# Optimization experiments

Measured on AMD Instinct MI355X. Metric: run time of the kernel, lower is better.

Reference implementation:

```python
import jax, jax.numpy as jnp
import numpy as np

N = 2048      # n_nodes
D = 512       # n_channels
AVG_DEG = 16  # average graph degree


def setup_inputs() -> dict:
    key = jax.random.key(0)
    k1, k2, k3 = jax.random.split(key, 3)
    # node features [N, D]
    x = jax.random.normal(k1, (N, D), dtype=jnp.float32)
    # random symmetric graph -> combinatorial Laplacian L = D - A
    E = N * AVG_DEG
    src = jax.random.randint(k2, (E,), 0, N)
    dst = jax.random.randint(k3, (E,), 0, N)
    A = jnp.zeros((N, N), jnp.float32).at[src, dst].add(1.0)
    A = (A + A.T) * 0.5
    A = A * (1.0 - jnp.eye(N, dtype=jnp.float32))  # drop self loops
    deg = A.sum(axis=1)
    L = jnp.diag(deg) - A
    # learned diffusion time (scalar parameter, ic=0.5)
    t = jnp.float32(0.5)
    return {"x": x, "L": L, "t": t}


def reference(x, L, t):
    # forward clamps diffusion_time to >= 1e-8
    tt = jnp.maximum(t, jnp.float32(1e-8))
    # heat kernel: expm(-t * L); the original loops over channels applying
    # compute_diffusion(x[:, [i]], t, L, 'matrix_exp') == expm(-t L) @ x[:, i],
    # which is exactly one dense matmul fused across all channels.
    P = jax.scipy.linalg.expm(-tt * L)  # [N, N]
    return P @ x  # [N, D]
```

## Files before the change

kernel.cpp:

```cpp
#include <hip/hip_runtime.h>

#define N_NODES 2048
#define N_CH    512
#define K_CHEB  48
#define NB      256

#define OFF_DIAG   0
#define OFF_BASE   20480
#define OFF_CNTO   28672
#define OFF_PKV    40960

#define PAD_OFF    16384u

__device__ __forceinline__ float b2f(unsigned short u) {
    return __uint_as_float(((unsigned int)u) << 16);
}
__device__ __forceinline__ bool detect32(const unsigned int* tw) {
    return (tw[0] & 0xFFFFu) == 0u;
}

__global__ void __launch_bounds__(256)
k_prep(const void* __restrict__ Lp, const unsigned int* __restrict__ tw,
       float* __restrict__ diagv, int* __restrict__ basev, int* __restrict__ cnto,
       unsigned short* __restrict__ pkv) {
    __shared__ unsigned short stage[4][N_NODES];
    __shared__ int scnt[4];
    int w    = threadIdx.x >> 6;
    int lane = threadIdx.x & 63;
    int row  = blockIdx.x * 4 + w;
    if (blockIdx.x == 0 && threadIdx.x == 0) diagv[N_NODES] = 0.f;
    bool is32 = detect32(tw);
    int run = 0; float dv = 0.f;
    if (is32) {
        const float4* rf4 = (const float4*)((const float*)Lp + (size_t)row * N_NODES);
        #pragma unroll
        for (int i = 0; i < 8; i++) {
            int j = i * 64 + lane;
            float4 v = rf4[j];
            if (j == (row >> 2)) {
                int rm = row & 3;
                if      (rm == 0) { dv = v.x; v.x = 0.f; }
                else if (rm == 1) { dv = v.y; v.y = 0.f; }
                else if (rm == 2) { dv = v.z; v.z = 0.f; }
                else              { dv = v.w; v.w = 0.f; }
            }
            int c0 = j * 4;
            int n0 = (v.x != 0.f) ? (int)(-2.0f * v.x + 0.5f) : 0;
            int n1 = (v.y != 0.f) ? (int)(-2.0f * v.y + 0.5f) : 0;
            int n2 = (v.z != 0.f) ? (int)(-2.0f * v.z + 0.5f) : 0;
            int n3 = (v.w != 0.f) ? (int)(-2.0f * v.w + 0.5f) : 0;
            int tn = n0 + n1 + n2 + n3;
            int xs = tn;
            #pragma unroll
            for (int d = 1; d < 64; d <<= 1) { int q = __shfl_up(xs, d); if (lane >= d) xs += q; }
            int o = run + xs - tn;
            for (int q = 0; q < n0; q++) stage[w][o++] = (unsigned short)((c0 + 0) << 3);
            for (int q = 0; q < n1; q++) stage[w][o++] = (unsigned short)((c0 + 1) << 3);
            for (int q = 0; q < n2; q++) stage[w][o++] = (unsigned short)((c0 + 2) << 3);
            for (int q = 0; q < n3; q++) stage[w][o++] = (unsigned short)((c0 + 3) << 3);
            run += __shfl(xs, 63);
        }
    } else {
        const unsigned short* rp = (const unsigned short*)Lp + (size_t)row * N_NODES;
        for (int c0 = 0; c0 < N_NODES; c0 += 64) {
            float v = b2f(rp[c0 + lane]);
            int n = 0;
            if (c0 + lane == row) dv = v;
            else if (v != 0.f)    n = (int)(-2.0f * v + 0.5f);
            int xs = n;
            #pragma unroll
            for (int d = 1; d < 64; d <<= 1) { int q = __shfl_up(xs, d); if (lane >= d) xs += q; }
            int o = run + xs - n;
            for (int q = 0; q < n; q++) stage[w][o + q] = (unsigned short)((c0 + lane) << 3);
            run += __shfl(xs, 63);
        }
    }
    #pragma unroll
    for (int o = 32; o; o >>= 1) dv += __shfl_xor(dv, o);
    int padded = (run + 7) & ~7;
    for (int e = run + lane; e < padded; e += 64) stage[w][e] = (unsigned short)PAD_OFF;
    if (lane == 0) scnt[w] = padded;
    __syncthreads();
    int myb = blockIdx.x * 256;
    for (int w2 = 0; w2 < w; w2++) myb += scnt[w2];
    if (lane == 0) { basev[row] = myb; cnto[row] = padded >> 3; diagv[row] = dv; }
    const unsigned int* s32 = (const unsigned int*)stage[w];
    unsigned int* p32 = (unsigned int*)pkv + (myb >> 1);
    for (int i = lane; i < (padded >> 1); i += 64) p32[i] = s32[i];
}

__device__ __forceinline__ void oct_acc(const float2* __restrict__ cur, uint4 q,
                                        float& ax, float& ay, float& bx, float& by) {
    const char* cb = (const char*)cur;
    #pragma unroll
    for (int i = 0; i < 4; i++) {
        unsigned int u = (i == 0) ? q.x : (i == 1) ? q.y : (i == 2) ? q.z : q.w;
        float2 c0 = *(const float2*)(cb + (u & 0xFFFFu));
        float2 c1 = *(const float2*)(cb + (u >> 16));
        ax += c0.x; ay += c0.y;
        bx += c1.x; by += c1.y;
    }
}

__device__ __forceinline__ float2 gatherR(const float2* __restrict__ cur,
                                          const uint4* __restrict__ s4,
                                          int j0, int j1) {
    float ax = 0.f, ay = 0.f, bx = 0.f, by = 0.f;
    int j = j0;
    if (j + 2 <= j1) {
        uint4 q0 = s4[j], q1 = s4[j + 1];
        j += 2;
        while (j + 2 <= j1) {
            uint4 p0 = s4[j], p1 = s4[j + 1];
            oct_acc(cur, q0, ax, ay, bx, by);
            oct_acc(cur, q1, ax, ay, bx, by);
            q0 = p0; q1 = p1;
            j += 2;
        }
        oct_acc(cur, q0, ax, ay, bx, by);
        oct_acc(cur, q1, ax, ay, bx, by);
    }
    if (j < j1) oct_acc(cur, s4[j], ax, ay, bx, by);
    return make_float2(ax + bx, ay + by);
}

__global__ void __launch_bounds__(1024, 4)
k_cheb(const void* __restrict__ x, const unsigned int* __restrict__ tw,
       const int* __restrict__ basev, const int* __restrict__ cnto,
       const float* __restrict__ diagv, const unsigned short* __restrict__ pkv,
       void* __restrict__ out) {
    __shared__ float2 bufA[N_NODES + 8];
    __shared__ float2 bufB[N_NODES + 8];
    __shared__ float  scoef[K_CHEB + 1];
    __shared__ float  cabs[K_CHEB + 1];
    __shared__ int    permL[N_NODES];
    __shared__ int    waveCnt[16][32];
    __shared__ int    wavePre[16][32];
    __shared__ int    hstart[32];
    __shared__ float  sred[16];
    __shared__ float  sredM[16];
    __shared__ double dzs;
    __shared__ float  gss;
    __shared__ int    kks;

    int t    = threadIdx.x;
    int lane = t & 63;
    int wid  = t >> 6;
    int cb   = ((blockIdx.x & 31) << 4) | ((blockIdx.x >> 5) << 1);
    bool is32 = detect32(tw);
    if (t == 0) {
        bufA[N_NODES] = make_float2(0.f, 0.f);
        bufB[N_NODES] = make_float2(0.f, 0.f);
    }
    float* dlds = (float*)bufA;
    int r0 = t, r1 = t + 1024;
    float d0v = diagv[r0], d1v = diagv[r1];
    dlds[r0] = d0v; dlds[r1] = d1v;
    if (t == 0) dlds[N_NODES] = 0.f;
    float mx = fmaxf(d0v, d1v);
    int q0 = min(cnto[r0], 31), q1 = min(cnto[r1], 31);
    unsigned long long below = (1ull << lane) - 1ull;
    int rk0 = 0, rk1 = 0;
    #pragma unroll 1
    for (int k = 0; k < 32; k++) {
        unsigned long long m0 = __ballot(q0 == k);
        unsigned long long m1 = __ballot(q1 == k);
        if (q0 == k) rk0 = (int)__popcll(m0 & below);
        if (q1 == k) rk1 = (int)__popcll(m0) + (int)__popcll(m1 & below);
        if (lane == 0) waveCnt[wid][k] = (int)(__popcll(m0) + __popcll(m1));
    }
    __syncthreads();
    float mb = 0.f;
    {
        const char* db = (const char*)dlds;
        const uint4* pk4 = (const uint4*)pkv;
        float s0 = 0.f, s1 = 0.f;
        int j0 = basev[r0] >> 3, n0 = cnto[r0];
        for (int j = 0; j < n0; j++) {
            uint4 q = pk4[j0 + j];
            s0 += *(const float*)(db + ((q.x & 0xFFFFu) >> 1)) + *(const float*)(db + (q.x >> 17))
                + *(const float*)(db + ((q.y & 0xFFFFu) >> 1)) + *(const float*)(db + (q.y >> 17))
                + *(const float*)(db + ((q.z & 0xFFFFu) >> 1)) + *(const float*)(db + (q.z >> 17))
                + *(const float*)(db + ((q.w & 0xFFFFu) >> 1)) + *(const float*)(db + (q.w >> 17));
        }
        int j1 = basev[r1] >> 3, n1 = cnto[r1];
        for (int j = 0; j < n1; j++) {
            uint4 q = pk4[j1 + j];
            s1 += *(const float*)(db + ((q.x & 0xFFFFu) >> 1)) + *(const float*)(db + (q.x >> 17))
                + *(const float*)(db + ((q.y & 0xFFFFu) >> 1)) + *(const float*)(db + (q.y >> 17))
                + *(const float*)(db + ((q.z & 0xFFFFu) >> 1)) + *(const float*)(db + (q.z >> 17))
                + *(const float*)(db + ((q.w & 0xFFFFu) >> 1)) + *(const float*)(db + (q.w >> 17));
        }
        if (d0v > 0.f) mb = d0v + 0.5f * s0 / d0v;
        if (d1v > 0.f) mb = fmaxf(mb, d1v + 0.5f * s1 / d1v);
    }
    #pragma unroll
    for (int o = 32; o; o >>= 1) {
        mx = fmaxf(mx, __shfl_xor(mx, o));
        mb = fmaxf(mb, __shfl_xor(mb, o));
    }
    if (lane == 0) { sred[wid] = mx; sredM[wid] = mb; }
    __syncthreads();
    if (t < 32) {
        int acc = 0;
        for (int w2 = 0; w2 < 16; w2++) { wavePre[w2][t] = acc; acc += waveCnt[w2][t]; }
        hstart[t] = acc;
    }
    __syncthreads();
    if (t == 0) {
        int acc = 0;
        for (int l = 31; l >= 0; l--) { int c = hstart[l]; hstart[l] = acc; acc += c; }
        float m = sred[0], mM = sredM[0];
        #pragma unroll
        for (int i = 1; i < 16; i++) { m = fmaxf(m, sred[i]); mM = fmaxf(mM, sredM[i]); }
        float tt = is32 ? __uint_as_float(tw[0]) : b2f((unsigned short)(tw[0] & 0xFFFFu));
        tt = fmaxf(tt, 1e-8f);
        float beta = 2.0f * m;
        float bM   = mM * 1.00002f + 1e-7f;
        if (bM > 0.f && bM < beta) beta = bM;
        gss = (beta > 0.f) ? 2.0f / beta : 0.f;
        dzs = (beta > 0.f) ? (double)tt * (double)beta * 0.5 : 0.0;
    }
    __syncthreads();
    if (t <= K_CHEB) {
        int k = t;
        double z = dzs;
        double emz = exp(-z), h = 0.5 * z, h2 = h * h;
        double term = 1.0;
        for (int j = 1; j <= k; j++) term *= h / (double)j;
        double sum = term;
        for (int m = 1; m < 300; m++) {
            term *= h2 / ((double)m * (double)(m + k));
            sum += term;
            if (term == 0.0 || term < sum * 1e-18) break;
        }
        double ck = emz * sum * (k == 0 ? 1.0 : 2.0);
        if (k & 1) ck = -ck;
        scoef[k] = (float)ck;
        cabs[k]  = (float)fabs(ck);
    }
    permL[hstart[q0] + wavePre[wid][q0] + rk0] = r0;
    permL[hstart[q1] + wavePre[wid][q1] + rk1] = r1;
    __syncthreads();
    if (t == 0) {
        int keff = 1;
        for (int k = K_CHEB; k >= 2; k--)
            if (cabs[k] >= 2.5e-4f) { keff = k; break; }
        kks = keff;
    }
    __syncthreads();

    int ra = permL[t], rb = permL[2047 - t];
    int na = cnto[ra], nb = cnto[rb];
    int ja = basev[ra] >> 3, jb = basev[rb] >> 3;
    const uint4* s4 = (const uint4*)pkv;
    float da = diagv[ra], db = diagv[rb];
    float g = gss;
    int   K = kks;

    float2 xa, xb;
    if (is32) {
        xa = *(const float2*)((const float*)x + (size_t)ra * N_CH + cb);
        xb = *(const float2*)((const float*)x + (size_t)rb * N_CH + cb);
    } else {
        const unsigned short* xp = (const unsigned short*)x;
        unsigned int wa = *(const unsigned int*)(xp + (size_t)ra * N_CH + cb);
        unsigned int wb = *(const unsigned int*)(xp + (size_t)rb * N_CH + cb);
        xa = make_float2(b2f((unsigned short)(wa & 0xFFFFu)), b2f((unsigned short)(wa >> 16)));
        xb = make_float2(b2f((unsigned short)(wb & 0xFFFFu)), b2f((unsigned short)(wb >> 16)));
    }
    bufA[ra] = xa; bufA[rb] = xb;
    __syncthreads();

    float gm = -0.5f * g;
    float ia = g * da - 1.f, ib = g * db - 1.f;
    float2 aa = gatherR(bufA, s4, ja, ja + na);
    float2 ab = gatherR(bufA, s4, jb, jb + nb);
    float2 pva = xa, pvb = xb;
    float2 cua = make_float2(gm * aa.x + ia * xa.x, gm * aa.y + ia * xa.y);
    float2 cub = make_float2(gm * ab.x + ib * xb.x, gm * ab.y + ib * xb.y);
    float c0 = scoef[0], c1 = scoef[1];
    float2 oa = make_float2(c0 * xa.x + c1 * cua.x, c0 * xa.y + c1 * cua.y);
    float2 ob = make_float2(c0 * xb.x + c1 * cub.x, c0 * xb.y + c1 * cub.y);
    bufB[ra] = cua; bufB[rb] = cub;
    __syncthreads();

    float gn  = -g;
    float dga = 2.f * g * da - 2.f, dgb = 2.f * g * db - 2.f;

#define CHEB_STEP(RD, WR)                                                  \
    {   float ck = scoef[k];                                               \
        float2 ba = gatherR(RD, s4, ja, ja + na);                          \
        float2 bb = gatherR(RD, s4, jb, jb + nb);                          \
        float2 tna = make_float2(gn * ba.x + dga * cua.x - pva.x,          \
                                 gn * ba.y + dga * cua.y - pva.y);         \
        float2 tnb = make_float2(gn * bb.x + dgb * cub.x - pvb.x,          \
                                 gn * bb.y + dgb * cub.y - pvb.y);         \
        pva = cua; cua = tna;                                              \
        pvb = cub; cub = tnb;                                              \
        oa.x += ck * tna.x; oa.y += ck * tna.y;                            \
        ob.x += ck * tnb.x; ob.y += ck * tnb.y;                            \
        WR[ra] = tna; WR[rb] = tnb;                                        \
        __syncthreads(); }

    int k = 2;
    while (k <= K) {
        CHEB_STEP(bufB, bufA)
        k++;
        if (k > K) break;
        CHEB_STEP(bufA, bufB)
        k++;
    }
#undef CHEB_STEP

    if (is32) {
        *(float2*)((float*)out + (size_t)ra * N_CH + cb) = oa;
        *(float2*)((float*)out + (size_t)rb * N_CH + cb) = ob;
    } else {
        unsigned int ua, ub;
        { unsigned int u0 = __float_as_uint(oa.x), u1 = __float_as_uint(oa.y);
          u0 = (u0 + 0x7FFFu + ((u0 >> 16) & 1u)) >> 16;
          u1 = (u1 + 0x7FFFu + ((u1 >> 16) & 1u)) >> 16;
          ua = u0 | (u1 << 16); }
        { unsigned int u0 = __float_as_uint(ob.x), u1 = __float_as_uint(ob.y);
          u0 = (u0 + 0x7FFFu + ((u0 >> 16) & 1u)) >> 16;
          u1 = (u1 + 0x7FFFu + ((u1 >> 16) & 1u)) >> 16;
          ub = u0 | (u1 << 16); }
        *(unsigned int*)((unsigned short*)out + (size_t)ra * N_CH + cb) = ua;
        *(unsigned int*)((unsigned short*)out + (size_t)rb * N_CH + cb) = ub;
    }
}

extern "C" void kernel_launch(void* const* d_in, const int* in_sizes, int n_in,
                              void* d_out, int out_size, void* d_ws, size_t ws_size,
                              hipStream_t stream) {
    const void* x  = d_in[0];
    const void* L  = d_in[1];
    const void* tp = d_in[2];
    const unsigned int* tw = (const unsigned int*)tp;

    char* ws = (char*)d_ws;
    float*          diagv = (float*)          (ws + OFF_DIAG);
    int*            basev = (int*)            (ws + OFF_BASE);
    int*            cnto  = (int*)            (ws + OFF_CNTO);
    unsigned short* pkv   = (unsigned short*) (ws + OFF_PKV);

    k_prep <<<512, 256, 0, stream>>>(L, tw, diagv, basev, cnto, pkv);
    k_cheb <<<NB, 1024, 0, stream>>>(x, tw, basev, cnto, diagv, pkv, d_out);
}
```

Baseline: 156.4 us.

## Fuse Laplacian packing and Chebyshev kernels via cooperative grid sync

Merges the sparse-packing prep kernel into the Chebyshev propagation kernel and launches the result as one cooperative kernel. A grid-wide sync separates the two phases. The staging buffer for packing reuses the shared memory that later holds the ping-pong vectors. This removes a kernel launch and the gap between the two kernels, at the cost of a grid barrier and of prep now running with only 8 of 16 waves per block active. It also needs all 256 blocks to be co-resident.

```diff
diff --git a/kernel.cpp b/kernel.cpp
--- a/kernel.cpp
+++ b/kernel.cpp
@@ -1,4 +1,7 @@
 #include <hip/hip_runtime.h>
+#include <hip/hip_cooperative_groups.h>
+
+namespace cg = cooperative_groups;
 
 #define N_NODES 2048
 #define N_CH    512
@@ -17,76 +20,6 @@
 }
 __device__ __forceinline__ bool detect32(const unsigned int* tw) {
     return (tw[0] & 0xFFFFu) == 0u;
-}
-
-__global__ void __launch_bounds__(256)
-k_prep(const void* __restrict__ Lp, const unsigned int* __restrict__ tw,
-       float* __restrict__ diagv, int* __restrict__ basev, int* __restrict__ cnto,
-       unsigned short* __restrict__ pkv) {
-    __shared__ unsigned short stage[4][N_NODES];
-    __shared__ int scnt[4];
-    int w    = threadIdx.x >> 6;
-    int lane = threadIdx.x & 63;
-    int row  = blockIdx.x * 4 + w;
-    if (blockIdx.x == 0 && threadIdx.x == 0) diagv[N_NODES] = 0.f;
-    bool is32 = detect32(tw);
-    int run = 0; float dv = 0.f;
-    if (is32) {
-        const float4* rf4 = (const float4*)((const float*)Lp + (size_t)row * N_NODES);
-        #pragma unroll
-        for (int i = 0; i < 8; i++) {
-            int j = i * 64 + lane;
-            float4 v = rf4[j];
-            if (j == (row >> 2)) {
-                int rm = row & 3;
-                if      (rm == 0) { dv = v.x; v.x = 0.f; }
-                else if (rm == 1) { dv = v.y; v.y = 0.f; }
-                else if (rm == 2) { dv = v.z; v.z = 0.f; }
-                else              { dv = v.w; v.w = 0.f; }
-            }
-            int c0 = j * 4;
-            int n0 = (v.x != 0.f) ? (int)(-2.0f * v.x + 0.5f) : 0;
-            int n1 = (v.y != 0.f) ? (int)(-2.0f * v.y + 0.5f) : 0;
-            int n2 = (v.z != 0.f) ? (int)(-2.0f * v.z + 0.5f) : 0;
-            int n3 = (v.w != 0.f) ? (int)(-2.0f * v.w + 0.5f) : 0;
-            int tn = n0 + n1 + n2 + n3;
-            int xs = tn;
-            #pragma unroll
-            for (int d = 1; d < 64; d <<= 1) { int q = __shfl_up(xs, d); if (lane >= d) xs += q; }
-            int o = run + xs - tn;
-            for (int q = 0; q < n0; q++) stage[w][o++] = (unsigned short)((c0 + 0) << 3);
-            for (int q = 0; q < n1; q++) stage[w][o++] = (unsigned short)((c0 + 1) << 3);
-            for (int q = 0; q < n2; q++) stage[w][o++] = (unsigned short)((c0 + 2) << 3);
-            for (int q = 0; q < n3; q++) stage[w][o++] = (unsigned short)((c0 + 3) << 3);
-            run += __shfl(xs, 63);
-        }
-    } else {
-        const unsigned short* rp = (const unsigned short*)Lp + (size_t)row * N_NODES;
-        for (int c0 = 0; c0 < N_NODES; c0 += 64) {
-            float v = b2f(rp[c0 + lane]);
-            int n = 0;
-            if (c0 + lane == row) dv = v;
-            else if (v != 0.f)    n = (int)(-2.0f * v + 0.5f);
-            int xs = n;
-            #pragma unroll
-            for (int d = 1; d < 64; d <<= 1) { int q = __shfl_up(xs, d); if (lane >= d) xs += q; }
-            int o = run + xs - n;
-            for (int q = 0; q < n; q++) stage[w][o + q] = (unsigned short)((c0 + lane) << 3);
-            run += __shfl(xs, 63);
-        }
-    }
-    #pragma unroll
-    for (int o = 32; o; o >>= 1) dv += __shfl_xor(dv, o);
-    int padded = (run + 7) & ~7;
-    for (int e = run + lane; e < padded; e += 64) stage[w][e] = (unsigned short)PAD_OFF;
-    if (lane == 0) scnt[w] = padded;
-    __syncthreads();
-    int myb = blockIdx.x * 256;
-    for (int w2 = 0; w2 < w; w2++) myb += scnt[w2];
-    if (lane == 0) { basev[row] = myb; cnto[row] = padded >> 3; diagv[row] = dv; }
-    const unsigned int* s32 = (const unsigned int*)stage[w];
-    unsigned int* p32 = (unsigned int*)pkv + (myb >> 1);
-    for (int i = lane; i < (padded >> 1); i += 64) p32[i] = s32[i];
 }
 
 __device__ __forceinline__ void oct_acc(const float2* __restrict__ cur, uint4 q,
@@ -125,12 +58,12 @@
 }
 
 __global__ void __launch_bounds__(1024, 4)
-k_cheb(const void* __restrict__ x, const unsigned int* __restrict__ tw,
-       const int* __restrict__ basev, const int* __restrict__ cnto,
-       const float* __restrict__ diagv, const unsigned short* __restrict__ pkv,
-       void* __restrict__ out) {
-    __shared__ float2 bufA[N_NODES + 8];
-    __shared__ float2 bufB[N_NODES + 8];
+k_all(const void* __restrict__ Lp, const void* __restrict__ x,
+      const unsigned int* __restrict__ tw,
+      float* __restrict__ diagv, int* __restrict__ basev, int* __restrict__ cnto,
+      unsigned short* __restrict__ pkv, void* __restrict__ out) {
+    __shared__ __align__(16) char smemAB[2 * (N_NODES + 8) * 8];
+    __shared__ int    scnt[8];
     __shared__ float  scoef[K_CHEB + 1];
     __shared__ float  cabs[K_CHEB + 1];
     __shared__ int    permL[N_NODES];
@@ -143,11 +76,81 @@
     __shared__ float  gss;
     __shared__ int    kks;
 
+    float2* bufA = (float2*)smemAB;
+    float2* bufB = bufA + (N_NODES + 8);
+
     int t    = threadIdx.x;
     int lane = t & 63;
     int wid  = t >> 6;
-    int cb   = ((blockIdx.x & 31) << 4) | ((blockIdx.x >> 5) << 1);
     bool is32 = detect32(tw);
+
+    int run = 0, padded = 0; float dv = 0.f;
+    int row = blockIdx.x * 8 + wid;
+    unsigned short* st = (unsigned short*)smemAB + wid * N_NODES;
+    if (wid < 8) {
+        if (is32) {
+            const float4* rf4 = (const float4*)((const float*)Lp + (size_t)row * N_NODES);
+            #pragma unroll
+            for (int i = 0; i < 8; i++) {
+                int j = i * 64 + lane;
+                float4 v = rf4[j];
+                if (j == (row >> 2)) {
+                    int rm = row & 3;
+                    if      (rm == 0) { dv = v.x; v.x = 0.f; }
+                    else if (rm == 1) { dv = v.y; v.y = 0.f; }
+                    else if (rm == 2) { dv = v.z; v.z = 0.f; }
+                    else              { dv = v.w; v.w = 0.f; }
+                }
+                int c0 = j * 4;
+                int n0 = (v.x != 0.f) ? (int)(-2.0f * v.x + 0.5f) : 0;
+                int n1 = (v.y != 0.f) ? (int)(-2.0f * v.y + 0.5f) : 0;
+                int n2 = (v.z != 0.f) ? (int)(-2.0f * v.z + 0.5f) : 0;
+                int n3 = (v.w != 0.f) ? (int)(-2.0f * v.w + 0.5f) : 0;
+                int tn = n0 + n1 + n2 + n3;
+                int xs = tn;
+                #pragma unroll
+                for (int d = 1; d < 64; d <<= 1) { int q = __shfl_up(xs, d); if (lane >= d) xs += q; }
+                int o = run + xs - tn;
+                for (int q = 0; q < n0; q++) st[o++] = (unsigned short)((c0 + 0) << 3);
+                for (int q = 0; q < n1; q++) st[o++] = (unsigned short)((c0 + 1) << 3);
+                for (int q = 0; q < n2; q++) st[o++] = (unsigned short)((c0 + 2) << 3);
+                for (int q = 0; q < n3; q++) st[o++] = (unsigned short)((c0 + 3) << 3);
+                run += __shfl(xs, 63);
+            }
+        } else {
+            const unsigned short* rp = (const unsigned short*)Lp + (size_t)row * N_NODES;
+            for (int c0 = 0; c0 < N_NODES; c0 += 64) {
+                float v = b2f(rp[c0 + lane]);
+                int n = 0;
+                if (c0 + lane == row) dv = v;
+                else if (v != 0.f)    n = (int)(-2.0f * v + 0.5f);
+                int xs = n;
+                #pragma unroll
+                for (int d = 1; d < 64; d <<= 1) { int q = __shfl_up(xs, d); if (lane >= d) xs += q; }
+                int o = run + xs - n;
+                for (int q = 0; q < n; q++) st[o + q] = (unsigned short)((c0 + lane) << 3);
+                run += __shfl(xs, 63);
+            }
+        }
+        #pragma unroll
+        for (int o = 32; o; o >>= 1) dv += __shfl_xor(dv, o);
+        padded = (run + 7) & ~7;
+        for (int e = run + lane; e < padded; e += 64) st[e] = (unsigned short)PAD_OFF;
+        if (lane == 0) scnt[wid] = padded;
+    }
+    __syncthreads();
+    if (wid < 8) {
+        int myb = blockIdx.x * 512;
+        for (int w2 = 0; w2 < wid; w2++) myb += scnt[w2];
+        if (lane == 0) { basev[row] = myb; cnto[row] = padded >> 3; diagv[row] = dv; }
+        const unsigned int* s32 = (const unsigned int*)st;
+        unsigned int* p32 = (unsigned int*)pkv + (myb >> 1);
+        for (int i = lane; i < (padded >> 1); i += 64) p32[i] = s32[i];
+    }
+    __threadfence();
+    cg::this_grid().sync();
+
+    int cb = ((blockIdx.x & 31) << 4) | ((blockIdx.x >> 5) << 1);
     if (t == 0) {
         bufA[N_NODES] = make_float2(0.f, 0.f);
         bufB[N_NODES] = make_float2(0.f, 0.f);
@@ -344,7 +347,10 @@
     int*            basev = (int*)            (ws + OFF_BASE);
     int*            cnto  = (int*)            (ws + OFF_CNTO);
     unsigned short* pkv   = (unsigned short*) (ws + OFF_PKV);
-
-    k_prep <<<512, 256, 0, stream>>>(L, tw, diagv, basev, cnto, pkv);
-    k_cheb <<<NB, 1024, 0, stream>>>(x, tw, basev, cnto, diagv, pkv, d_out);
-}
+    void*           outp  = d_out;
+
+    void* kargs[] = { (void*)&L, (void*)&x, (void*)&tw, (void*)&diagv,
+                      (void*)&basev, (void*)&cnto, (void*)&pkv, (void*)&outp };
+    hipLaunchCooperativeKernel((const void*)k_all, dim3(NB), dim3(1024),
+                               kargs, 0, stream);
+}
```

Result: slower. 275.5 us (+76.2%).
